# Kernel optimization log

Hardware: AMD Instinct MI355X
Metric: run time of the kernel (lower is better)

The kernel has to match this reference:

```python
import jax, jax.numpy as jnp
import numpy as np

N_NODES = 100000
N_EDGES = 3200000
F_IN, F_HID, F_OUT = 512, 128, 32


def setup_inputs() -> dict:
    key = jax.random.key(0)
    ks = jax.random.split(key, 8)
    x = jax.random.normal(ks[0], (N_NODES, F_IN), dtype=jnp.float32)
    edge_row = jax.random.randint(ks[1], (N_EDGES,), 0, N_NODES, dtype=jnp.int32)
    edge_col = jax.random.randint(ks[2], (N_EDGES,), 0, N_NODES, dtype=jnp.int32)
    edge_val = jax.random.uniform(ks[3], (N_EDGES,), dtype=jnp.float32)
    W1 = jax.random.normal(ks[4], (F_IN, F_HID), dtype=jnp.float32) / np.sqrt(F_IN)
    b1 = jnp.zeros((F_HID,), dtype=jnp.float32)
    W2 = jax.random.normal(ks[5], (F_HID, F_OUT), dtype=jnp.float32) / np.sqrt(F_HID)
    b2 = jnp.zeros((F_OUT,), dtype=jnp.float32)
    return {"x": x, "edge_row": edge_row, "edge_col": edge_col,
            "edge_val": edge_val, "W1": W1, "b1": b1, "W2": W2, "b2": b2}


def _spmm(edge_row, edge_col, edge_val, dense):
    # out[r] = sum_{e: row[e]==r} val[e] * dense[col[e]]  (COO SpMM)
    gathered = dense[edge_col] * edge_val[:, None]  # [E, F]
    return jax.ops.segment_sum(gathered, edge_row, num_segments=N_NODES)


def reference(x, edge_row, edge_col, edge_val, W1, b1, W2, b2):
    # GraphConvolution 1: support = x@W1; out = A @ support + b1
    h = _spmm(edge_row, edge_col, edge_val, x @ W1) + b1
    h = jax.nn.relu(h)
    # GraphConvolution 2
    logits = _spmm(edge_row, edge_col, edge_val, h @ W2) + b2
    return jax.nn.log_softmax(logits, axis=1)
```

## Files before the change

kernel.cpp:

```cpp
#include <hip/hip_runtime.h>


#define NN 100000
#define NE 3200000
#define FIN 512
#define FHID 128
#define FOUT 32
#define BROWS 64
#define NBUCK 1563
#define NPART 512
#define CHUNK 6250
#define TOT (NBUCK * NPART)
#define NSCAN1 782
#define GG1 ((NN + 127) / 128)

typedef __attribute__((ext_vector_type(8))) short bf16x8;
typedef __attribute__((ext_vector_type(4))) float f32x4;

static __device__ __forceinline__ unsigned short f2bf(float f) {
    unsigned u = __float_as_uint(f);
    unsigned r = (u + 0x7FFFu + ((u >> 16) & 1u)) >> 16;
    return (unsigned short)r;
}
static __device__ __forceinline__ float bf2f(unsigned short u) {
    return __uint_as_float(((unsigned)u) << 16);
}
static __device__ __forceinline__ float bflo(unsigned u) {
    return __uint_as_float(u << 16);
}
static __device__ __forceinline__ float bfhi(unsigned u) {
    return __uint_as_float(u & 0xffff0000u);
}

__global__ __launch_bounds__(256) void fused_prep_hist(const float* __restrict__ W1,
                                                       unsigned short* __restrict__ W1t,
                                                       const int* __restrict__ erow,
                                                       int* __restrict__ cntG) {
    if (blockIdx.x < NPART) {
        __shared__ int c[NBUCK];
        const int t = threadIdx.x;
        const int w = blockIdx.x;
        for (int i = t; i < NBUCK; i += 256) c[i] = 0;
        __syncthreads();
        const int e0 = w * CHUNK;
        const int e1 = min(e0 + CHUNK, NE);
        for (int e = e0 + t; e < e1; e += 256) atomicAdd(&c[erow[e] >> 6], 1);
        __syncthreads();
        for (int i = t; i < NBUCK; i += 256) cntG[w * NBUCK + i] = c[i];
    } else {
        int t = (blockIdx.x - NPART) * 256 + threadIdx.x;
        int n = t & 127;
        int k = t >> 7;
        W1t[n * 512 + k] = f2bf(W1[k * 128 + n]);
    }
}

__global__ __launch_bounds__(256) void scan1_kernel(const int* __restrict__ cntG,
                                                    int* __restrict__ off,
                                                    int* __restrict__ partials) {
    __shared__ int s[256];
    int t = threadIdx.x;
    int i0 = blockIdx.x * 1024 + t * 4;
    int v[4];
#pragma unroll
    for (int j = 0; j < 4; ++j) {
        int i = i0 + j;
        v[j] = (i < TOT) ? cntG[(i & (NPART - 1)) * NBUCK + (i >> 9)] : 0;
    }
    int lsum = v[0] + v[1] + v[2] + v[3];
    s[t] = lsum;
    __syncthreads();
    for (int o = 1; o < 256; o <<= 1) {
        int xv = (t >= o) ? s[t - o] : 0;
        __syncthreads();
        s[t] += xv;
        __syncthreads();
    }
    if (t == 255) partials[blockIdx.x] = s[255];
    int run = s[t] - lsum;
#pragma unroll
    for (int j = 0; j < 4; ++j) {
        if (i0 + j < TOT) off[i0 + j] = run;
        run += v[j];
    }
}

__global__ __launch_bounds__(1024) void scan2_kernel(int* partials) {
    __shared__ int s[1024];
    int t = threadIdx.x;
    int v = (t < NSCAN1) ? partials[t] : 0;
    s[t] = v;
    __syncthreads();
    for (int o = 1; o < 1024; o <<= 1) {
        int xv = (t >= o) ? s[t - o] : 0;
        __syncthreads();
        s[t] += xv;
        __syncthreads();
    }
    if (t < NSCAN1) partials[t] = s[t] - v;
}

__global__ __launch_bounds__(256) void scan3_kernel(int* __restrict__ off,
                                                    const int* __restrict__ partials) {
    int add = partials[blockIdx.x];
    int i0 = blockIdx.x * 1024 + threadIdx.x * 4;
#pragma unroll
    for (int j = 0; j < 4; ++j)
        if (i0 + j < TOT) off[i0 + j] += add;
}

__global__ __launch_bounds__(256) void scatter_part(const int* __restrict__ erow,
                                                    const int* __restrict__ ecol,
                                                    const float* __restrict__ eval,
                                                    const int* __restrict__ off,
                                                    int2* __restrict__ bcolval) {
    __shared__ int pos[NBUCK];
    const int t = threadIdx.x;
    const int w = blockIdx.x;
    for (int b = t; b < NBUCK; b += 256) pos[b] = off[b * NPART + w];
    __syncthreads();
    const int e0 = w * CHUNK;
    const int e1 = min(e0 + CHUNK, NE);
    for (int e = e0 + t; e < e1; e += 256) {
        int r = erow[e];
        int idx = atomicAdd(&pos[r >> 6], 1);
        bcolval[idx] = make_int2(ecol[e] | ((r & 63) << 20), __float_as_int(eval[e]));
    }
}

__global__ __launch_bounds__(256) void fused_csr_gemm1(
    const int* __restrict__ off, const int2* __restrict__ bcolval,
    int* __restrict__ rowptr, int2* __restrict__ epack,
    const float* __restrict__ x, const unsigned short* __restrict__ W1t,
    unsigned short* __restrict__ outd) {
    if (blockIdx.x >= NBUCK) {
        __shared__ __align__(16) unsigned short As[128 * 32];
        const int tid = threadIdx.x;
        const int lane = tid & 63;
        const int w = __builtin_amdgcn_readfirstlane(tid >> 6);
        const int quad = lane >> 4;
        const int m = lane & 15;
        const int row0 = (blockIdx.x - NBUCK) * 128;

        f32x4 acc[8][2];
#pragma unroll
        for (int mt = 0; mt < 8; ++mt)
#pragma unroll
            for (int nt = 0; nt < 2; ++nt) acc[mt][nt] = (f32x4){0.f, 0.f, 0.f, 0.f};

        int srow[4], skq[4];
        const float* sptr[4];
#pragma unroll
        for (int s = 0; s < 4; ++s) {
            int f = tid + s * 256;
            srow[s] = f >> 3;
            skq[s] = f & 7;
            sptr[s] = x + (size_t)(row0 + srow[s]) * FIN + skq[s] * 4;
        }
        float4 ld[4];
#pragma unroll
        for (int s = 0; s < 4; ++s)
            ld[s] = (row0 + srow[s] < NN) ? *(const float4*)sptr[s]
                                          : make_float4(0.f, 0.f, 0.f, 0.f);

        for (int ks = 0; ks < 16; ++ks) {
            __syncthreads();
#pragma unroll
            for (int s = 0; s < 4; ++s) {
                int r = srow[s], kq = skq[s];
                int mt = r >> 4, mm = r & 15;
                int offs = mt * 512 + (kq >> 1) * 128 + mm * 8 + (kq & 1) * 4;
                ushort4 p;
                p.x = f2bf(ld[s].x);
                p.y = f2bf(ld[s].y);
                p.z = f2bf(ld[s].z);
                p.w = f2bf(ld[s].w);
                *(ushort4*)&As[offs] = p;
            }
            __syncthreads();
            if (ks < 15) {
#pragma unroll
                for (int s = 0; s < 4; ++s)
                    ld[s] = (row0 + srow[s] < NN)
                                ? *(const float4*)(sptr[s] + (ks + 1) * 32)
                                : make_float4(0.f, 0.f, 0.f, 0.f);
            }
            bf16x8 bfr[2];
#pragma unroll
            for (int nt = 0; nt < 2; ++nt) {
                int n = (w * 2 + nt) * 16 + m;
                bfr[nt] = *(const bf16x8*)(W1t + (size_t)n * 512 + ks * 32 + quad * 8);
            }
#pragma unroll
            for (int mt = 0; mt < 8; ++mt) {
                bf16x8 af = *(const bf16x8*)&As[mt * 512 + quad * 128 + m * 8];
                acc[mt][0] = __builtin_amdgcn_mfma_f32_16x16x32_bf16(af, bfr[0], acc[mt][0], 0, 0, 0);
                acc[mt][1] = __builtin_amdgcn_mfma_f32_16x16x32_bf16(af, bfr[1], acc[mt][1], 0, 0, 0);
            }
        }
#pragma unroll
        for (int mt = 0; mt < 8; ++mt)
#pragma unroll
            for (int nt = 0; nt < 2; ++nt) {
                int col = (w * 2 + nt) * 16 + m;
#pragma unroll
                for (int r = 0; r < 4; ++r) {
                    int row = row0 + mt * 16 + quad * 4 + r;
                    if (row < NN) outd[(size_t)row * FHID + col] = f2bf(acc[mt][nt][r]);
                }
            }
    } else {
        __shared__ int cnt[BROWS];
        __shared__ int pos[BROWS];
        __shared__ int s[BROWS];
        const int b = blockIdx.x;
        const int t = threadIdx.x;
        const int s0 = off[b * NPART];
        const int send = (b == NBUCK - 1) ? NE : off[(b + 1) * NPART];
        const int n = send - s0;
        if (t < BROWS) cnt[t] = 0;
        __syncthreads();
        for (int i = t; i < n; i += 256)
            atomicAdd(&cnt[((unsigned)bcolval[s0 + i].x) >> 20], 1);
        __syncthreads();
        int myc = (t < BROWS) ? cnt[t] : 0;
        if (t < BROWS) s[t] = myc;
        __syncthreads();
        for (int o = 1; o < BROWS; o <<= 1) {
            int xv = (t >= o && t < BROWS) ? s[t - o] : 0;
            __syncthreads();
            if (t < BROWS) s[t] += xv;
            __syncthreads();
        }
        if (t < BROWS) {
            int excl = s[t] - myc;
            pos[t] = excl;
            int row = b * BROWS + t;
            if (row < NN) rowptr[row] = s0 + excl;
        }
        if (b == 0 && t == 0) rowptr[NN] = NE;
        __syncthreads();
        for (int i = t; i < n; i += 256) {
            int2 v = bcolval[s0 + i];
            int p = atomicAdd(&pos[((unsigned)v.x) >> 20], 1);
            epack[s0 + p] = make_int2(v.x & 0xFFFFF, v.y);
        }
    }
}

__global__ __launch_bounds__(256) void spmm1_kernel(const int* __restrict__ rowptr,
                                                    const int2* __restrict__ epack,
                                                    const unsigned short* __restrict__ dense,
                                                    const float* __restrict__ b1,
                                                    unsigned short* __restrict__ h) {
    const int lane = threadIdx.x & 63;
    const int row = blockIdx.x * 4 + (threadIdx.x >> 6);
    const int start = __builtin_amdgcn_readfirstlane(rowptr[row]);
    const int cnt = __builtin_amdgcn_readfirstlane(rowptr[row + 1]) - start;
    const int sl16 = lane & 15;
    float acc0 = 0.f, acc1 = 0.f;

    for (int j = 0; j < cnt; j += 16) {
        int idx = j + sl16;
        idx = idx < cnt ? idx : cnt - 1;
        const int2 p = epack[start + idx];
        const int rem = cnt - j;
        unsigned d[16];
#pragma unroll
        for (int k = 0; k < 16; ++k) {
            int col = __builtin_amdgcn_readlane(p.x, k);
            col = (k < rem) ? col : 0;
            d[k] = *((const unsigned*)(dense + ((size_t)col << 7)) + lane);
        }
#pragma unroll
        for (int k = 0; k < 16; ++k) {
            float v = (k < rem) ? __int_as_float(__builtin_amdgcn_readlane(p.y, k)) : 0.f;
            acc0 = fmaf(v, bflo(d[k]), acc0);
            acc1 = fmaf(v, bfhi(d[k]), acc1);
        }
    }
    float2 bb = *(const float2*)(b1 + lane * 2);
    unsigned r0 = f2bf(fmaxf(acc0 + bb.x, 0.f));
    unsigned r1 = f2bf(fmaxf(acc1 + bb.y, 0.f));
    *((unsigned*)(h + (size_t)row * FHID) + lane) = r0 | (r1 << 16);
}

__global__ __launch_bounds__(256) void gemm2_kernel(const unsigned short* __restrict__ h,
                                                    const float* __restrict__ W2,
                                                    unsigned short* __restrict__ out) {
    __shared__ float hs[64][129];
    const int tid = threadIdx.x;
    const int lane = tid & 63;
    const int cg = __builtin_amdgcn_readfirstlane(tid >> 6);
    const int row0 = blockIdx.x * 64;
    const int row = row0 + lane;

    float acc[8];
#pragma unroll
    for (int c = 0; c < 8; ++c) acc[c] = 0.f;

#pragma unroll
    for (int j = 0; j < 8; ++j) {
        int f4 = tid + j * 256;
        int r = f4 >> 5;
        int kq = f4 & 31;
        ushort4 v = make_ushort4(0, 0, 0, 0);
        if (row0 + r < NN) v = *(const ushort4*)(h + (size_t)(row0 + r) * FHID + kq * 4);
        hs[r][kq * 4 + 0] = bf2f(v.x);
        hs[r][kq * 4 + 1] = bf2f(v.y);
        hs[r][kq * 4 + 2] = bf2f(v.z);
        hs[r][kq * 4 + 3] = bf2f(v.w);
    }
    __syncthreads();
#pragma unroll 4
    for (int k = 0; k < FHID; ++k) {
        float a = hs[lane][k];
        const float* wrow = W2 + k * FOUT + cg * 8;
#pragma unroll
        for (int c = 0; c < 8; ++c) acc[c] += a * wrow[c];
    }
    if (row < NN) {
        uint4 st;
        st.x = (unsigned)f2bf(acc[0]) | ((unsigned)f2bf(acc[1]) << 16);
        st.y = (unsigned)f2bf(acc[2]) | ((unsigned)f2bf(acc[3]) << 16);
        st.z = (unsigned)f2bf(acc[4]) | ((unsigned)f2bf(acc[5]) << 16);
        st.w = (unsigned)f2bf(acc[6]) | ((unsigned)f2bf(acc[7]) << 16);
        *(uint4*)(out + (size_t)row * FOUT + cg * 8) = st;
    }
}

__global__ __launch_bounds__(256) void spmm2_kernel(const int* __restrict__ rowptr,
                                                    const int2* __restrict__ epack,
                                                    const unsigned short* __restrict__ dense,
                                                    const float* __restrict__ b2,
                                                    float* __restrict__ out) {
    const int lane = threadIdx.x & 63;
    const int row = blockIdx.x * 4 + (threadIdx.x >> 6);
    const int start = __builtin_amdgcn_readfirstlane(rowptr[row]);
    const int cnt = __builtin_amdgcn_readfirstlane(rowptr[row + 1]) - start;
    const int col = lane & 31;
    const int slot = lane >> 5;
    const int sl16 = lane & 15;
    float acc = 0.f;

    for (int j = 0; j < cnt; j += 16) {
        int idx = j + sl16;
        idx = idx < cnt ? idx : cnt - 1;
        const int2 p = epack[start + idx];
        const int rem = cnt - j;
        unsigned short d[8];
        float vv[8];
#pragma unroll
        for (int k = 0; k < 8; ++k) {
            int cA = __builtin_amdgcn_readlane(p.x, 2 * k);
            int cB = __builtin_amdgcn_readlane(p.x, 2 * k + 1);
            int ei = 2 * k + slot;
            int c = slot ? cB : cA;
            c = (ei < rem) ? c : 0;
            d[k] = *(dense + (size_t)c * FOUT + col);
            int vA = __builtin_amdgcn_readlane(p.y, 2 * k);
            int vB = __builtin_amdgcn_readlane(p.y, 2 * k + 1);
            float v = __int_as_float(slot ? vB : vA);
            vv[k] = (ei < rem) ? v : 0.f;
        }
#pragma unroll
        for (int k = 0; k < 8; ++k) acc = fmaf(vv[k], bf2f(d[k]), acc);
    }
    acc += __shfl_xor(acc, 32, 64);
    acc += b2[col];
    float m = acc;
#pragma unroll
    for (int mask = 16; mask >= 1; mask >>= 1) m = fmaxf(m, __shfl_xor(m, mask, 64));
    float ex = expf(acc - m);
    float ssum = ex;
#pragma unroll
    for (int mask = 16; mask >= 1; mask >>= 1) ssum += __shfl_xor(ssum, mask, 64);
    float lse = m + logf(ssum);
    if (lane < 32) out[(size_t)row * FOUT + col] = acc - lse;
}

extern "C" void kernel_launch(void* const* d_in, const int* in_sizes, int n_in,
                              void* d_out, int out_size, void* d_ws, size_t ws_size,
                              hipStream_t stream) {
    const float* x = (const float*)d_in[0];
    const int* erow = (const int*)d_in[1];
    const int* ecol = (const int*)d_in[2];
    const float* eval = (const float*)d_in[3];
    const float* W1 = (const float*)d_in[4];
    const float* b1 = (const float*)d_in[5];
    const float* W2 = (const float*)d_in[6];
    const float* b2 = (const float*)d_in[7];
    float* out = (float*)d_out;

    char* ws = (char*)d_ws;
    size_t off_b = 0;
    auto walloc = [&](size_t bytes) -> void* {
        void* p = ws + off_b;
        off_b = (off_b + bytes + 255) & ~(size_t)255;
        return p;
    };
    int2* epack = (int2*)walloc((size_t)NE * 8);
    int* rowptr = (int*)walloc((size_t)(NN + 1) * 4);
    int* cntG = (int*)walloc((size_t)TOT * 4);
    int* off = (int*)walloc((size_t)TOT * 4);
    int* partials = (int*)walloc(4096);
    unsigned short* W1t = (unsigned short*)walloc((size_t)FHID * FIN * 2);
    int2* bcolval = (int2*)walloc((size_t)NE * 8);
    unsigned short* support1 = (unsigned short*)walloc((size_t)NN * FHID * 2);
    unsigned short* h = (unsigned short*)walloc((size_t)NN * FHID * 2);
    unsigned short* support2 = support1;

    fused_prep_hist<<<NPART + 256, 256, 0, stream>>>(W1, W1t, erow, cntG);
    scan1_kernel<<<NSCAN1, 256, 0, stream>>>(cntG, off, partials);
    scan2_kernel<<<1, 1024, 0, stream>>>(partials);
    scan3_kernel<<<NSCAN1, 256, 0, stream>>>(off, partials);
    scatter_part<<<NPART, 256, 0, stream>>>(erow, ecol, eval, off, bcolval);
    fused_csr_gemm1<<<NBUCK + GG1, 256, 0, stream>>>(off, bcolval, rowptr, epack,
                                                     x, W1t, support1);
    spmm1_kernel<<<NN / 4, 256, 0, stream>>>(rowptr, epack, support1, b1, h);
    gemm2_kernel<<<(NN + 63) / 64, 256, 0, stream>>>(h, W2, support2);
    spmm2_kernel<<<NN / 4, 256, 0, stream>>>(rowptr, epack, support2, b2, out);
}
```

Baseline: 663.7 us.

## Split fused CSR/GEMM1 kernel; LDS-staged bucket sort and register-direct MFMA GEMM

Splits the fused CSR-build plus GEMM1 kernel into two launches. The bucket-to-CSR kernel now keeps bucket entries in registers and sorts them through a shared-memory buffer so the epack writes are coalesced, falling back to the old path for oversized buckets. GEMM1 drops the LDS staging of x: each wave loads its A fragments straight from global memory with prefetching. W1t is pre-laid out in MFMA fragment order so B fragments load contiguously. The split gives up the overlap between CSR build and GEMM and adds one launch, and each wave now reads all of W1t.

```diff
diff --git a/kernel.cpp b/kernel.cpp
--- a/kernel.cpp
+++ b/kernel.cpp
@@ -12,7 +12,7 @@
 #define CHUNK 6250
 #define TOT (NBUCK * NPART)
 #define NSCAN1 782
-#define GG1 ((NN + 127) / 128)
+#define EBCAP 2560
 
 typedef __attribute__((ext_vector_type(8))) short bf16x8;
 typedef __attribute__((ext_vector_type(4))) float f32x4;
@@ -30,6 +30,14 @@
 }
 static __device__ __forceinline__ float bfhi(unsigned u) {
     return __uint_as_float(u & 0xffff0000u);
+}
+static __device__ __forceinline__ bf16x8 pack8(float4 u, float4 v) {
+    bf16x8 r;
+    r[0] = (short)f2bf(u.x); r[1] = (short)f2bf(u.y);
+    r[2] = (short)f2bf(u.z); r[3] = (short)f2bf(u.w);
+    r[4] = (short)f2bf(v.x); r[5] = (short)f2bf(v.y);
+    r[6] = (short)f2bf(v.z); r[7] = (short)f2bf(v.w);
+    return r;
 }
 
 __global__ __launch_bounds__(256) void fused_prep_hist(const float* __restrict__ W1,
@@ -49,9 +57,14 @@
         for (int i = t; i < NBUCK; i += 256) cntG[w * NBUCK + i] = c[i];
     } else {
         int t = (blockIdx.x - NPART) * 256 + threadIdx.x;
-        int n = t & 127;
-        int k = t >> 7;
-        W1t[n * 512 + k] = f2bf(W1[k * 128 + n]);
+        int j = t & 7;
+        int c = t >> 3;
+        int l = c & 63;
+        int ks = (c >> 6) & 15;
+        int nt = c >> 10;
+        int n = nt * 16 + (l & 15);
+        int k = ks * 32 + ((l >> 4) << 3) + j;
+        W1t[(size_t)c * 8 + j] = f2bf(W1[k * FHID + n]);
     }
 }
 
@@ -128,124 +141,138 @@
     }
 }
 
-__global__ __launch_bounds__(256) void fused_csr_gemm1(
-    const int* __restrict__ off, const int2* __restrict__ bcolval,
-    int* __restrict__ rowptr, int2* __restrict__ epack,
-    const float* __restrict__ x, const unsigned short* __restrict__ W1t,
-    unsigned short* __restrict__ outd) {
-    if (blockIdx.x >= NBUCK) {
-        __shared__ __align__(16) unsigned short As[128 * 32];
-        const int tid = threadIdx.x;
-        const int lane = tid & 63;
-        const int w = __builtin_amdgcn_readfirstlane(tid >> 6);
-        const int quad = lane >> 4;
-        const int m = lane & 15;
-        const int row0 = (blockIdx.x - NBUCK) * 128;
-
-        f32x4 acc[8][2];
-#pragma unroll
-        for (int mt = 0; mt < 8; ++mt)
-#pragma unroll
-            for (int nt = 0; nt < 2; ++nt) acc[mt][nt] = (f32x4){0.f, 0.f, 0.f, 0.f};
-
-        int srow[4], skq[4];
-        const float* sptr[4];
-#pragma unroll
-        for (int s = 0; s < 4; ++s) {
-            int f = tid + s * 256;
-            srow[s] = f >> 3;
-            skq[s] = f & 7;
-            sptr[s] = x + (size_t)(row0 + srow[s]) * FIN + skq[s] * 4;
-        }
-        float4 ld[4];
-#pragma unroll
-        for (int s = 0; s < 4; ++s)
-            ld[s] = (row0 + srow[s] < NN) ? *(const float4*)sptr[s]
-                                          : make_float4(0.f, 0.f, 0.f, 0.f);
-
-        for (int ks = 0; ks < 16; ++ks) {
-            __syncthreads();
-#pragma unroll
-            for (int s = 0; s < 4; ++s) {
-                int r = srow[s], kq = skq[s];
-                int mt = r >> 4, mm = r & 15;
-                int offs = mt * 512 + (kq >> 1) * 128 + mm * 8 + (kq & 1) * 4;
-                ushort4 p;
-                p.x = f2bf(ld[s].x);
-                p.y = f2bf(ld[s].y);
-                p.z = f2bf(ld[s].z);
-                p.w = f2bf(ld[s].w);
-                *(ushort4*)&As[offs] = p;
+__global__ __launch_bounds__(256) void bucket_to_csr(const int* __restrict__ off,
+                                                     const int2* __restrict__ bcolval,
+                                                     int* __restrict__ rowptr,
+                                                     int2* __restrict__ epack) {
+    __shared__ int cnt[BROWS];
+    __shared__ int pos[BROWS];
+    __shared__ int s[BROWS];
+    __shared__ int2 eb[EBCAP];
+    const int b = blockIdx.x;
+    const int t = threadIdx.x;
+    const int s0 = off[b * NPART];
+    const int send = (b == NBUCK - 1) ? NE : off[(b + 1) * NPART];
+    const int n = send - s0;
+    const bool fits = (n <= EBCAP);
+    if (t < BROWS) cnt[t] = 0;
+    __syncthreads();
+    int2 myv[10];
+    if (fits) {
+#pragma unroll
+        for (int ii = 0; ii < 10; ++ii) {
+            int i = t + ii * 256;
+            int2 v = make_int2(0, 0);
+            if (i < n) {
+                v = bcolval[s0 + i];
+                atomicAdd(&cnt[((unsigned)v.x) >> 20], 1);
             }
-            __syncthreads();
-            if (ks < 15) {
-#pragma unroll
-                for (int s = 0; s < 4; ++s)
-                    ld[s] = (row0 + srow[s] < NN)
-                                ? *(const float4*)(sptr[s] + (ks + 1) * 32)
-                                : make_float4(0.f, 0.f, 0.f, 0.f);
-            }
-            bf16x8 bfr[2];
-#pragma unroll
-            for (int nt = 0; nt < 2; ++nt) {
-                int n = (w * 2 + nt) * 16 + m;
-                bfr[nt] = *(const bf16x8*)(W1t + (size_t)n * 512 + ks * 32 + quad * 8);
-            }
-#pragma unroll
-            for (int mt = 0; mt < 8; ++mt) {
-                bf16x8 af = *(const bf16x8*)&As[mt * 512 + quad * 128 + m * 8];
-                acc[mt][0] = __builtin_amdgcn_mfma_f32_16x16x32_bf16(af, bfr[0], acc[mt][0], 0, 0, 0);
-                acc[mt][1] = __builtin_amdgcn_mfma_f32_16x16x32_bf16(af, bfr[1], acc[mt][1], 0, 0, 0);
-            }
-        }
-#pragma unroll
-        for (int mt = 0; mt < 8; ++mt)
-#pragma unroll
-            for (int nt = 0; nt < 2; ++nt) {
-                int col = (w * 2 + nt) * 16 + m;
-#pragma unroll
-                for (int r = 0; r < 4; ++r) {
-                    int row = row0 + mt * 16 + quad * 4 + r;
-                    if (row < NN) outd[(size_t)row * FHID + col] = f2bf(acc[mt][nt][r]);
-                }
-            }
+            myv[ii] = v;
+        }
     } else {
-        __shared__ int cnt[BROWS];
-        __shared__ int pos[BROWS];
-        __shared__ int s[BROWS];
-        const int b = blockIdx.x;
-        const int t = threadIdx.x;
-        const int s0 = off[b * NPART];
-        const int send = (b == NBUCK - 1) ? NE : off[(b + 1) * NPART];
-        const int n = send - s0;
-        if (t < BROWS) cnt[t] = 0;
-        __syncthreads();
         for (int i = t; i < n; i += 256)
             atomicAdd(&cnt[((unsigned)bcolval[s0 + i].x) >> 20], 1);
-        __syncthreads();
-        int myc = (t < BROWS) ? cnt[t] : 0;
-        if (t < BROWS) s[t] = myc;
-        __syncthreads();
-        for (int o = 1; o < BROWS; o <<= 1) {
-            int xv = (t >= o && t < BROWS) ? s[t - o] : 0;
-            __syncthreads();
-            if (t < BROWS) s[t] += xv;
-            __syncthreads();
-        }
-        if (t < BROWS) {
-            int excl = s[t] - myc;
-            pos[t] = excl;
-            int row = b * BROWS + t;
-            if (row < NN) rowptr[row] = s0 + excl;
-        }
-        if (b == 0 && t == 0) rowptr[NN] = NE;
-        __syncthreads();
+    }
+    __syncthreads();
+    int myc = (t < BROWS) ? cnt[t] : 0;
+    if (t < BROWS) s[t] = myc;
+    __syncthreads();
+    for (int o = 1; o < BROWS; o <<= 1) {
+        int xv = (t >= o && t < BROWS) ? s[t - o] : 0;
+        __syncthreads();
+        if (t < BROWS) s[t] += xv;
+        __syncthreads();
+    }
+    if (t < BROWS) {
+        int excl = s[t] - myc;
+        pos[t] = excl;
+        int row = b * BROWS + t;
+        if (row < NN) rowptr[row] = s0 + excl;
+    }
+    if (b == 0 && t == 0) rowptr[NN] = NE;
+    __syncthreads();
+    if (fits) {
+#pragma unroll
+        for (int ii = 0; ii < 10; ++ii) {
+            int i = t + ii * 256;
+            if (i < n) {
+                int2 v = myv[ii];
+                int p = atomicAdd(&pos[((unsigned)v.x) >> 20], 1);
+                eb[p] = make_int2(v.x & 0xFFFFF, v.y);
+            }
+        }
+        __syncthreads();
+        for (int i = t; i < n; i += 256) epack[s0 + i] = eb[i];
+    } else {
         for (int i = t; i < n; i += 256) {
             int2 v = bcolval[s0 + i];
             int p = atomicAdd(&pos[((unsigned)v.x) >> 20], 1);
             epack[s0 + p] = make_int2(v.x & 0xFFFFF, v.y);
         }
     }
+}
+
+__global__ __launch_bounds__(256) void gemm1_mfma(const float* __restrict__ x,
+                                                  const unsigned short* __restrict__ W1t,
+                                                  unsigned short* __restrict__ out) {
+    const int tid = threadIdx.x;
+    const int lane = tid & 63;
+    const int w = tid >> 6;
+    const int quad = lane >> 4;
+    const int m = lane & 15;
+    const int row0 = blockIdx.x * 128 + w * 32;
+
+    int rA = row0 + m;
+    int rB = row0 + 16 + m;
+    rA = rA < NN ? rA : NN - 1;
+    rB = rB < NN ? rB : NN - 1;
+    const float* pA = x + (size_t)rA * FIN + quad * 8;
+    const float* pB = x + (size_t)rB * FIN + quad * 8;
+
+    f32x4 acc[2][8];
+#pragma unroll
+    for (int i = 0; i < 2; ++i)
+#pragma unroll
+        for (int nt = 0; nt < 8; ++nt) acc[i][nt] = (f32x4){0.f, 0.f, 0.f, 0.f};
+
+    float4 a0 = *(const float4*)pA;
+    float4 a1 = *(const float4*)(pA + 4);
+    float4 b0 = *(const float4*)pB;
+    float4 b1 = *(const float4*)(pB + 4);
+
+    for (int ks = 0; ks < 16; ++ks) {
+        const int kn = (ks + 1) & 15;
+        float4 na0 = *(const float4*)(pA + kn * 32);
+        float4 na1 = *(const float4*)(pA + kn * 32 + 4);
+        float4 nb0 = *(const float4*)(pB + kn * 32);
+        float4 nb1 = *(const float4*)(pB + kn * 32 + 4);
+
+        bf16x8 fA = pack8(a0, a1);
+        bf16x8 fB = pack8(b0, b1);
+        bf16x8 bb[8];
+#pragma unroll
+        for (int nt = 0; nt < 8; ++nt)
+            bb[nt] = *(const bf16x8*)(W1t + ((size_t)((nt * 16 + ks) * 64 + lane)) * 8);
+#pragma unroll
+        for (int nt = 0; nt < 8; ++nt) {
+            acc[0][nt] = __builtin_amdgcn_mfma_f32_16x16x32_bf16(fA, bb[nt], acc[0][nt], 0, 0, 0);
+            acc[1][nt] = __builtin_amdgcn_mfma_f32_16x16x32_bf16(fB, bb[nt], acc[1][nt], 0, 0, 0);
+        }
+        a0 = na0; a1 = na1; b0 = nb0; b1 = nb1;
+    }
+
+    const int crow0 = blockIdx.x * 128 + w * 32;
+#pragma unroll
+    for (int i = 0; i < 2; ++i)
+#pragma unroll
+        for (int nt = 0; nt < 8; ++nt) {
+            int col = nt * 16 + m;
+#pragma unroll
+            for (int r = 0; r < 4; ++r) {
+                int row = crow0 + i * 16 + quad * 4 + r;
+                if (row < NN) out[(size_t)row * FHID + col] = f2bf(acc[i][nt][r]);
+            }
+        }
 }
 
 __global__ __launch_bounds__(256) void spmm1_kernel(const int* __restrict__ rowptr,
@@ -415,8 +442,8 @@
     scan2_kernel<<<1, 1024, 0, stream>>>(partials);
     scan3_kernel<<<NSCAN1, 256, 0, stream>>>(off, partials);
     scatter_part<<<NPART, 256, 0, stream>>>(erow, ecol, eval, off, bcolval);
-    fused_csr_gemm1<<<NBUCK + GG1, 256, 0, stream>>>(off, bcolval, rowptr, epack,
-                                                     x, W1t, support1);
+    bucket_to_csr<<<NBUCK, 256, 0, stream>>>(off, bcolval, rowptr, epack);
+    gemm1_mfma<<<(NN + 127) / 128, 256, 0, stream>>>(x, W1t, support1);
     spmm1_kernel<<<NN / 4, 256, 0, stream>>>(rowptr, epack, support1, b1, h);
     gemm2_kernel<<<(NN + 63) / 64, 256, 0, stream>>>(h, W2, support2);
     spmm2_kernel<<<NN / 4, 256, 0, stream>>>(rowptr, epack, support2, b2, out);
```

Measured after the change: 657.1 us. About the same (-1.0%).
